# Kernel tuning notes

Hardware: AMD Instinct MI355X
Metric: run time of the kernel (lower is better)

## Reference

```python
import jax, jax.numpy as jnp
import numpy as np

NUM_HEADS = 16
BIG_NEG = -1e9  # additive mask value for padded keys (fp32)


def setup_inputs() -> dict:
    key = jax.random.key(0)
    ks = jax.random.split(key, 12)
    T, S, B, E = 2048, 2048, 2, 1024
    bound = np.sqrt(6.0 / (E + E))  # xavier_uniform for square E x E weights
    inp = {
        'query': jax.random.normal(ks[0], (T, B, E), jnp.float32),
        'key': jax.random.normal(ks[1], (S, B, E), jnp.float32),
        'value': jax.random.normal(ks[2], (S, B, E), jnp.float32),
        'attn_mask': jax.random.normal(ks[3], (T, S), jnp.float32) * 0.1,
        'key_padding_mask': jnp.zeros((B, S), dtype=bool),
        'Wq': jax.random.uniform(ks[4], (E, E), jnp.float32, -bound, bound),
        'bq': jnp.zeros((E,), jnp.float32),
        'Wk': jax.random.uniform(ks[5], (E, E), jnp.float32, -bound, bound),
        'bk': jnp.zeros((E,), jnp.float32),
        'Wv': jax.random.uniform(ks[6], (E, E), jnp.float32, -bound, bound),
        'bv': jnp.zeros((E,), jnp.float32),
        'Wo': jax.random.uniform(ks[7], (E, E), jnp.float32, -bound, bound),
        'bo': jnp.zeros((E,), jnp.float32),
    }
    return inp


def reference(query, key, value, attn_mask, key_padding_mask,
              Wq, bq, Wk, bk, Wv, bv, Wo, bo):
    T, B, E = query.shape
    S = key.shape[0]
    H = NUM_HEADS
    d = E // H
    scale = 1.0 / jnp.sqrt(jnp.asarray(d, query.dtype))

    # projections (nn.Linear: x @ W.T + b), then split heads
    q = (query @ Wq.T + bq).reshape(T, B, H, d) * scale  # [T,B,H,d]
    k = (key @ Wk.T + bk).reshape(S, B, H, d)            # [S,B,H,d]
    v = (value @ Wv.T + bv).reshape(S, B, H, d)          # [S,B,H,d]

    # QK^T scores: [B,H,T,S]
    scores = jnp.einsum('tbhd,sbhd->bhts', q, k)

    # merge masks: additive attn_mask + key_padding_mask (True -> -inf)
    merged = attn_mask[None, None, :, :] + jnp.where(
        key_padding_mask[:, None, None, :], BIG_NEG, 0.0).astype(scores.dtype)
    scores = scores + merged

    attn = jax.nn.softmax(scores, axis=-1)  # dropout p=0 -> identity

    out = jnp.einsum('bhts,sbhd->tbhd', attn, v).reshape(T, B, E)
    return out @ Wo.T + bo  # [T,B,E]
```

## Files before the change

### kernel.cpp

```cpp
#include <hip/hip_runtime.h>
#include <hip/hip_bf16.h>

typedef unsigned short u16;
typedef __attribute__((ext_vector_type(8))) short bf16x8;
typedef __attribute__((ext_vector_type(4))) float f32x4;

#define T_DIM 2048
#define S_DIM 2048
#define B_DIM 2
#define E_DIM 1024
#define H_DIM 16
#define D_HEAD 64
#define NTOK 4096

#if __has_builtin(__builtin_amdgcn_exp2f)
#define EXP2F(x) __builtin_amdgcn_exp2f(x)
#else
#define EXP2F(x) exp2f(x)
#endif

__device__ __forceinline__ float bf2f(u16 u) {
  union { unsigned int i; float f; } v; v.i = ((unsigned int)u) << 16; return v.f;
}
__device__ __forceinline__ u16 f2bf(float f) {
  union { float f; unsigned int i; } v; v.f = f;
  unsigned int r = v.i + 0x7fffu + ((v.i >> 16) & 1u);
  return (u16)(r >> 16);
}
__device__ __forceinline__ unsigned pk2(float a, float b) {
  return (unsigned)f2bf(a) | ((unsigned)f2bf(b) << 16);
}
__device__ __forceinline__ float bfu_lo(unsigned w) {
  union { unsigned int i; float f; } v; v.i = w << 16; return v.f;
}
__device__ __forceinline__ float bfu_hi(unsigned w) {
  union { unsigned int i; float f; } v; v.i = w & 0xffff0000u; return v.f;
}
__device__ __forceinline__ uint4 loadA8(const void* A, size_t base, int bf) {
  if (bf) return *(const uint4*)&((const u16*)A)[base];
  const float* af = (const float*)A + base;
  uint4 r;
  r.x = pk2(af[0], af[1]); r.y = pk2(af[2], af[3]);
  r.z = pk2(af[4], af[5]); r.w = pk2(af[6], af[7]);
  return r;
}

__global__ void detect_dtype(const u16* q, int* flag) {
  int lane = threadIdx.x;
  float v = bf2f(q[2 * lane]);
  bool ok = (v < 16.f) && (v > -16.f);
  unsigned long long b = __ballot(ok);
  if (lane == 0) *flag = (b == ~0ull) ? 1 : 0;
}

__global__ void prep_params(const void* Wq, const void* Wk, const void* Wv, const void* Wo,
                            const void* bq, const void* bk, const void* bv, const void* bo,
                            u16* wqkv, u16* wo, float* b3, float* bof,
                            const int* flag) {
  const int bf = *flag;
  const int W = E_DIM * E_DIM;
  int idx = blockIdx.x * 256 + threadIdx.x;
  if (idx < 4 * W) {
    int which = idx / W, i = idx - which * W;
    const void* src = which == 0 ? Wq : which == 1 ? Wk : which == 2 ? Wv : Wo;
    float v = bf ? bf2f(((const u16*)src)[i]) : ((const float*)src)[i];
    if (which == 0) v *= 0.125f;
    if (which < 3) wqkv[idx] = f2bf(v);
    else           wo[i] = f2bf(v);
  } else {
    int j = idx - 4 * W;
    if (j < 4 * E_DIM) {
      int which = j / E_DIM, i = j - which * E_DIM;
      const void* src = which == 0 ? bq : which == 1 ? bk : which == 2 ? bv : bo;
      float v = bf ? bf2f(((const u16*)src)[i]) : ((const float*)src)[i];
      if (which == 0) v *= 0.125f;
      if (which < 3) b3[j] = v;
      else           bof[i] = v;
    }
  }
}

__launch_bounds__(256)
__global__ void conv_in(const void* __restrict__ Q, const void* __restrict__ K,
                        const void* __restrict__ V,
                        u16* __restrict__ qb, u16* __restrict__ kb,
                        u16* __restrict__ vb, const int* __restrict__ flag) {
  const int bf = *flag;
  const size_t W = (size_t)NTOK * E_DIM;
  size_t e8 = ((size_t)blockIdx.x * 256 + threadIdx.x) * 8;
  int which = (int)(e8 / W);
  size_t i = e8 - (size_t)which * W;
  const void* src = which == 0 ? Q : which == 1 ? K : V;
  u16* dst = which == 0 ? qb : which == 1 ? kb : vb;
  *(uint4*)&dst[i] = loadA8(src, i, bf);
}

__global__ void prep_mask(const void* mask, const unsigned char* kpm,
                          u16* Mc, const int* flag) {
  const float L2E = 1.44269504f;
  const int bf = *flag;
  size_t e8 = ((size_t)blockIdx.x * 256 + threadIdx.x) * 8;
  int b = (int)(e8 / ((size_t)T_DIM * S_DIM));
  size_t rem = e8 - (size_t)b * T_DIM * S_DIM;
  int t = (int)(rem / S_DIM), s = (int)(rem - (size_t)t * S_DIM);
  const unsigned char* kb = &kpm[(size_t)b * S_DIM + s];
  uint4 o;
  if (bf) {
    const u16* m8 = &((const u16*)mask)[(size_t)t * S_DIM + s];
    o.x = pk2((bf2f(m8[0]) + (kb[0] ? -1e9f : 0.f)) * L2E,
              (bf2f(m8[1]) + (kb[1] ? -1e9f : 0.f)) * L2E);
    o.y = pk2((bf2f(m8[2]) + (kb[2] ? -1e9f : 0.f)) * L2E,
              (bf2f(m8[3]) + (kb[3] ? -1e9f : 0.f)) * L2E);
    o.z = pk2((bf2f(m8[4]) + (kb[4] ? -1e9f : 0.f)) * L2E,
              (bf2f(m8[5]) + (kb[5] ? -1e9f : 0.f)) * L2E);
    o.w = pk2((bf2f(m8[6]) + (kb[6] ? -1e9f : 0.f)) * L2E,
              (bf2f(m8[7]) + (kb[7] ? -1e9f : 0.f)) * L2E);
  } else {
    const float* mf = (const float*)mask + (size_t)t * S_DIM + s;
    o.x = pk2((mf[0] + (kb[0] ? -1e9f : 0.f)) * L2E,
              (mf[1] + (kb[1] ? -1e9f : 0.f)) * L2E);
    o.y = pk2((mf[2] + (kb[2] ? -1e9f : 0.f)) * L2E,
              (mf[3] + (kb[3] ? -1e9f : 0.f)) * L2E);
    o.z = pk2((mf[4] + (kb[4] ? -1e9f : 0.f)) * L2E,
              (mf[5] + (kb[5] ? -1e9f : 0.f)) * L2E);
    o.w = pk2((mf[6] + (kb[6] ? -1e9f : 0.f)) * L2E,
              (mf[7] + (kb[7] ? -1e9f : 0.f)) * L2E);
  }
  *(uint4*)&Mc[e8] = o;
}

__launch_bounds__(256)
__global__ void transpose_v(const u16* __restrict__ vp, u16* __restrict__ vt) {
  __shared__ unsigned int t[64 * 65];
  const int tid = threadIdx.x;
  const int s0 = blockIdx.x * 64;
  const int bh = blockIdx.y;
  const int b = bh / H_DIM, h = bh % H_DIM;
  {
    int sr = tid >> 2, cq = (tid & 3) * 16;
    const u16* src = &vp[((size_t)(s0 + sr) * B_DIM + b) * E_DIM + h * 64 + cq];
#pragma unroll
    for (int j = 0; j < 16; j++) t[(cq + j) * 65 + sr] = src[j];
  }
  __syncthreads();
  {
    int d = tid >> 2, sq = (tid & 3) * 16;
    u16* dst = &vt[((size_t)bh * 64 + d) * S_DIM + s0 + sq];
    uint4 o0, o1;
    o0.x = (t[d*65+sq+0] & 0xffffu) | (t[d*65+sq+1] << 16);
    o0.y = (t[d*65+sq+2] & 0xffffu) | (t[d*65+sq+3] << 16);
    o0.z = (t[d*65+sq+4] & 0xffffu) | (t[d*65+sq+5] << 16);
    o0.w = (t[d*65+sq+6] & 0xffffu) | (t[d*65+sq+7] << 16);
    o1.x = (t[d*65+sq+8] & 0xffffu) | (t[d*65+sq+9] << 16);
    o1.y = (t[d*65+sq+10] & 0xffffu) | (t[d*65+sq+11] << 16);
    o1.z = (t[d*65+sq+12] & 0xffffu) | (t[d*65+sq+13] << 16);
    o1.w = (t[d*65+sq+14] & 0xffffu) | (t[d*65+sq+15] << 16);
    *(uint4*)&dst[0] = o0;
    *(uint4*)&dst[8] = o1;
  }
}

__launch_bounds__(256, 2)
__global__ void gemm_qkv(const u16* __restrict__ Qb2, const u16* __restrict__ Kb2,
                         const u16* __restrict__ Vb2, const u16* __restrict__ W3,
                         const float* __restrict__ b3,
                         u16* __restrict__ qp, u16* __restrict__ kp, u16* __restrict__ vp) {
  __shared__ alignas(16) u16 As[128 * 72];
  __shared__ alignas(16) u16 Bs[128 * 72];
  const int tid = threadIdx.x;
  const int wave = tid >> 6, lane = tid & 63;
  const int g = lane >> 4, c = lane & 15;
  const int wy = wave >> 1, wx = wave & 1;
  const int which = blockIdx.x >> 3;
  const u16* A = which == 0 ? Qb2 : which == 1 ? Kb2 : Vb2;
  u16* dst = which == 0 ? qp : which == 1 ? kp : vp;
  const int m0 = blockIdx.y * 128, n0 = blockIdx.x * 128;
  const int K = E_DIM;
  const int rr = tid >> 3, oo = (tid & 7) * 8;

  uint4 pa0, pa1, pa2, pa3, pb0, pb1, pb2, pb3;
  pa0 = *(const uint4*)&A[(size_t)(m0 + rr)      * K + oo];
  pa1 = *(const uint4*)&A[(size_t)(m0 + rr + 32) * K + oo];
  pa2 = *(const uint4*)&A[(size_t)(m0 + rr + 64) * K + oo];
  pa3 = *(const uint4*)&A[(size_t)(m0 + rr + 96) * K + oo];
  pb0 = *(const uint4*)&W3[(size_t)(n0 + rr)      * K + oo];
  pb1 = *(const uint4*)&W3[(size_t)(n0 + rr + 32) * K + oo];
  pb2 = *(const uint4*)&W3[(size_t)(n0 + rr + 64) * K + oo];
  pb3 = *(const uint4*)&W3[(size_t)(n0 + rr + 96) * K + oo];

  f32x4 acc[4][4] = {};
  for (int kc = 0; kc < K; kc += 64) {
    *(uint4*)&As[(rr)      * 72 + oo] = pa0;
    *(uint4*)&As[(rr + 32) * 72 + oo] = pa1;
    *(uint4*)&As[(rr + 64) * 72 + oo] = pa2;
    *(uint4*)&As[(rr + 96) * 72 + oo] = pa3;
    *(uint4*)&Bs[(rr)      * 72 + oo] = pb0;
    *(uint4*)&Bs[(rr + 32) * 72 + oo] = pb1;
    *(uint4*)&Bs[(rr + 64) * 72 + oo] = pb2;
    *(uint4*)&Bs[(rr + 96) * 72 + oo] = pb3;
    __syncthreads();
    if (kc + 64 < K) {
      int k2 = kc + 64;
      pa0 = *(const uint4*)&A[(size_t)(m0 + rr)      * K + k2 + oo];
      pa1 = *(const uint4*)&A[(size_t)(m0 + rr + 32) * K + k2 + oo];
      pa2 = *(const uint4*)&A[(size_t)(m0 + rr + 64) * K + k2 + oo];
      pa3 = *(const uint4*)&A[(size_t)(m0 + rr + 96) * K + k2 + oo];
      pb0 = *(const uint4*)&W3[(size_t)(n0 + rr)      * K + k2 + oo];
      pb1 = *(const uint4*)&W3[(size_t)(n0 + rr + 32) * K + k2 + oo];
      pb2 = *(const uint4*)&W3[(size_t)(n0 + rr + 64) * K + k2 + oo];
      pb3 = *(const uint4*)&W3[(size_t)(n0 + rr + 96) * K + k2 + oo];
    }
#pragma unroll
    for (int ks = 0; ks < 2; ks++) {
      bf16x8 av0 = *(const bf16x8*)&As[(wy * 64 + 0 * 16 + c) * 72 + ks * 32 + g * 8];
      bf16x8 av1 = *(const bf16x8*)&As[(wy * 64 + 1 * 16 + c) * 72 + ks * 32 + g * 8];
      bf16x8 av2 = *(const bf16x8*)&As[(wy * 64 + 2 * 16 + c) * 72 + ks * 32 + g * 8];
      bf16x8 av3 = *(const bf16x8*)&As[(wy * 64 + 3 * 16 + c) * 72 + ks * 32 + g * 8];
      bf16x8 bv0 = *(const bf16x8*)&Bs[(wx * 64 + 0 * 16 + c) * 72 + ks * 32 + g * 8];
      bf16x8 bv1 = *(const bf16x8*)&Bs[(wx * 64 + 1 * 16 + c) * 72 + ks * 32 + g * 8];
      bf16x8 bv2 = *(const bf16x8*)&Bs[(wx * 64 + 2 * 16 + c) * 72 + ks * 32 + g * 8];
      bf16x8 bv3 = *(const bf16x8*)&Bs[(wx * 64 + 3 * 16 + c) * 72 + ks * 32 + g * 8];
      acc[0][0] = __builtin_amdgcn_mfma_f32_16x16x32_bf16(av0, bv0, acc[0][0], 0, 0, 0);
      acc[0][1] = __builtin_amdgcn_mfma_f32_16x16x32_bf16(av0, bv1, acc[0][1], 0, 0, 0);
      acc[0][2] = __builtin_amdgcn_mfma_f32_16x16x32_bf16(av0, bv2, acc[0][2], 0, 0, 0);
      acc[0][3] = __builtin_amdgcn_mfma_f32_16x16x32_bf16(av0, bv3, acc[0][3], 0, 0, 0);
      acc[1][0] = __builtin_amdgcn_mfma_f32_16x16x32_bf16(av1, bv0, acc[1][0], 0, 0, 0);
      acc[1][1] = __builtin_amdgcn_mfma_f32_16x16x32_bf16(av1, bv1, acc[1][1], 0, 0, 0);
      acc[1][2] = __builtin_amdgcn_mfma_f32_16x16x32_bf16(av1, bv2, acc[1][2], 0, 0, 0);
      acc[1][3] = __builtin_amdgcn_mfma_f32_16x16x32_bf16(av1, bv3, acc[1][3], 0, 0, 0);
      acc[2][0] = __builtin_amdgcn_mfma_f32_16x16x32_bf16(av2, bv0, acc[2][0], 0, 0, 0);
      acc[2][1] = __builtin_amdgcn_mfma_f32_16x16x32_bf16(av2, bv1, acc[2][1], 0, 0, 0);
      acc[2][2] = __builtin_amdgcn_mfma_f32_16x16x32_bf16(av2, bv2, acc[2][2], 0, 0, 0);
      acc[2][3] = __builtin_amdgcn_mfma_f32_16x16x32_bf16(av2, bv3, acc[2][3], 0, 0, 0);
      acc[3][0] = __builtin_amdgcn_mfma_f32_16x16x32_bf16(av3, bv0, acc[3][0], 0, 0, 0);
      acc[3][1] = __builtin_amdgcn_mfma_f32_16x16x32_bf16(av3, bv1, acc[3][1], 0, 0, 0);
      acc[3][2] = __builtin_amdgcn_mfma_f32_16x16x32_bf16(av3, bv2, acc[3][2], 0, 0, 0);
      acc[3][3] = __builtin_amdgcn_mfma_f32_16x16x32_bf16(av3, bv3, acc[3][3], 0, 0, 0);
    }
    __syncthreads();
  }
#pragma unroll
  for (int mi = 0; mi < 4; mi++)
#pragma unroll
    for (int ni = 0; ni < 4; ni++)
#pragma unroll
      for (int r = 0; r < 4; r++) {
        int row = m0 + wy * 64 + mi * 16 + g * 4 + r;
        int col = n0 + wx * 64 + ni * 16 + c;
        int inner = col & (E_DIM - 1);
        dst[(size_t)row * E_DIM + inner] = f2bf(acc[mi][ni][r] + b3[col]);
      }
}

__launch_bounds__(256, 2)
__global__ void gemm_o(const u16* __restrict__ A, const u16* __restrict__ Bw,
                       const float* __restrict__ bias, void* __restrict__ C,
                       int out_f32) {
  __shared__ alignas(16) u16 As[64 * 72];
  __shared__ alignas(16) u16 Bs[128 * 72];
  const int tid = threadIdx.x;
  const int wave = tid >> 6, lane = tid & 63;
  const int g = lane >> 4, c = lane & 15;
  const int wy = wave >> 1, wx = wave & 1;
  const int m0 = blockIdx.y * 64, n0 = blockIdx.x * 128;
  const int K = E_DIM, N = E_DIM;
  const int rr = tid >> 3, oo = (tid & 7) * 8;

  uint4 pa0, pa1, pb0, pb1, pb2, pb3;
  pa0 = *(const uint4*)&A[(size_t)(m0 + rr)      * K + oo];
  pa1 = *(const uint4*)&A[(size_t)(m0 + rr + 32) * K + oo];
  pb0 = *(const uint4*)&Bw[(size_t)(n0 + rr)      * K + oo];
  pb1 = *(const uint4*)&Bw[(size_t)(n0 + rr + 32) * K + oo];
  pb2 = *(const uint4*)&Bw[(size_t)(n0 + rr + 64) * K + oo];
  pb3 = *(const uint4*)&Bw[(size_t)(n0 + rr + 96) * K + oo];

  f32x4 acc[2][4] = {};
  for (int kc = 0; kc < K; kc += 64) {
    *(uint4*)&As[(rr)      * 72 + oo] = pa0;
    *(uint4*)&As[(rr + 32) * 72 + oo] = pa1;
    *(uint4*)&Bs[(rr)      * 72 + oo] = pb0;
    *(uint4*)&Bs[(rr + 32) * 72 + oo] = pb1;
    *(uint4*)&Bs[(rr + 64) * 72 + oo] = pb2;
    *(uint4*)&Bs[(rr + 96) * 72 + oo] = pb3;
    __syncthreads();
    if (kc + 64 < K) {
      int k2 = kc + 64;
      pa0 = *(const uint4*)&A[(size_t)(m0 + rr)      * K + k2 + oo];
      pa1 = *(const uint4*)&A[(size_t)(m0 + rr + 32) * K + k2 + oo];
      pb0 = *(const uint4*)&Bw[(size_t)(n0 + rr)      * K + k2 + oo];
      pb1 = *(const uint4*)&Bw[(size_t)(n0 + rr + 32) * K + k2 + oo];
      pb2 = *(const uint4*)&Bw[(size_t)(n0 + rr + 64) * K + k2 + oo];
      pb3 = *(const uint4*)&Bw[(size_t)(n0 + rr + 96) * K + k2 + oo];
    }
#pragma unroll
    for (int ks = 0; ks < 2; ks++) {
      bf16x8 av0 = *(const bf16x8*)&As[(wy * 32 + 0 * 16 + c) * 72 + ks * 32 + g * 8];
      bf16x8 av1 = *(const bf16x8*)&As[(wy * 32 + 1 * 16 + c) * 72 + ks * 32 + g * 8];
      bf16x8 bv0 = *(const bf16x8*)&Bs[(wx * 64 + 0 * 16 + c) * 72 + ks * 32 + g * 8];
      bf16x8 bv1 = *(const bf16x8*)&Bs[(wx * 64 + 1 * 16 + c) * 72 + ks * 32 + g * 8];
      bf16x8 bv2 = *(const bf16x8*)&Bs[(wx * 64 + 2 * 16 + c) * 72 + ks * 32 + g * 8];
      bf16x8 bv3 = *(const bf16x8*)&Bs[(wx * 64 + 3 * 16 + c) * 72 + ks * 32 + g * 8];
      acc[0][0] = __builtin_amdgcn_mfma_f32_16x16x32_bf16(av0, bv0, acc[0][0], 0, 0, 0);
      acc[0][1] = __builtin_amdgcn_mfma_f32_16x16x32_bf16(av0, bv1, acc[0][1], 0, 0, 0);
      acc[0][2] = __builtin_amdgcn_mfma_f32_16x16x32_bf16(av0, bv2, acc[0][2], 0, 0, 0);
      acc[0][3] = __builtin_amdgcn_mfma_f32_16x16x32_bf16(av0, bv3, acc[0][3], 0, 0, 0);
      acc[1][0] = __builtin_amdgcn_mfma_f32_16x16x32_bf16(av1, bv0, acc[1][0], 0, 0, 0);
      acc[1][1] = __builtin_amdgcn_mfma_f32_16x16x32_bf16(av1, bv1, acc[1][1], 0, 0, 0);
      acc[1][2] = __builtin_amdgcn_mfma_f32_16x16x32_bf16(av1, bv2, acc[1][2], 0, 0, 0);
      acc[1][3] = __builtin_amdgcn_mfma_f32_16x16x32_bf16(av1, bv3, acc[1][3], 0, 0, 0);
    }
    __syncthreads();
  }
#pragma unroll
  for (int mi = 0; mi < 2; mi++)
#pragma unroll
    for (int ni = 0; ni < 4; ni++)
#pragma unroll
      for (int r = 0; r < 4; r++) {
        int row = m0 + wy * 32 + mi * 16 + g * 4 + r;
        int col = n0 + wx * 64 + ni * 16 + c;
        float v = acc[mi][ni][r] + bias[col];
        size_t idx = (size_t)row * N + col;
        if (out_f32) ((float*)C)[idx] = v;
        else         ((u16*)C)[idx] = f2bf(v);
      }
}

__launch_bounds__(256, 4)
__global__ void flash_attn(const u16* __restrict__ Qb, const u16* __restrict__ Kb,
                           const u16* __restrict__ Vtg, const u16* __restrict__ Mc,
                           u16* __restrict__ ctx) {
  __shared__ alignas(16) u16 Ks[64 * 72];
  __shared__ alignas(16) u16 Vs[64 * 72];
  __shared__ alignas(16) u16 MP[64 * 72];
  const int tid = threadIdx.x;
  const int wave = tid >> 6, lane = tid & 63;
  const int g = lane >> 4, c = lane & 15;
  const int bh = blockIdx.x;
  const int t0 = blockIdx.y * 64;
  const int b = bh / H_DIM, h = bh % H_DIM;
  const size_t hoff = (size_t)h * D_HEAD;
  const float L2E = 1.44269504f;
  const u16* mc = &Mc[((size_t)b * T_DIM + t0) * S_DIM];
  const int rr = tid >> 3, oo = (tid & 7) * 8;

  *(uint4*)&Ks[(rr)      * 72 + oo] =
      *(const uint4*)&Qb[((size_t)(t0 + rr)      * B_DIM + b) * E_DIM + hoff + oo];
  *(uint4*)&Ks[(rr + 32) * 72 + oo] =
      *(const uint4*)&Qb[((size_t)(t0 + rr + 32) * B_DIM + b) * E_DIM + hoff + oo];
  __syncthreads();
  const int arow = wave * 16 + c;
  bf16x8 q0 = *(const bf16x8*)&Ks[arow * 72 + g * 8];
  bf16x8 q1 = *(const bf16x8*)&Ks[arow * 72 + 32 + g * 8];

  uint4 pk0, pk1, pv0, pv1, pm0, pm1;
  pk0 = *(const uint4*)&Kb[((size_t)(rr)      * B_DIM + b) * E_DIM + hoff + oo];
  pk1 = *(const uint4*)&Kb[((size_t)(rr + 32) * B_DIM + b) * E_DIM + hoff + oo];
  pv0 = *(const uint4*)&Vtg[((size_t)bh * 64 + rr)      * S_DIM + oo];
  pv1 = *(const uint4*)&Vtg[((size_t)bh * 64 + rr + 32) * S_DIM + oo];
  pm0 = *(const uint4*)&mc[(size_t)(rr)      * S_DIM + oo];
  pm1 = *(const uint4*)&mc[(size_t)(rr + 32) * S_DIM + oo];
  __syncthreads();

  f32x4 O[4] = {};
  float rsum = 0.f;
  const int trow = arow * 72;

  for (int s0 = 0; s0 < S_DIM; s0 += 64) {
    *(uint4*)&Ks[(rr)      * 72 + oo] = pk0;
    *(uint4*)&Ks[(rr + 32) * 72 + oo] = pk1;
    *(uint4*)&Vs[(rr)      * 72 + oo] = pv0;
    *(uint4*)&Vs[(rr + 32) * 72 + oo] = pv1;
    *(uint4*)&MP[(rr)      * 72 + oo] = pm0;
    *(uint4*)&MP[(rr + 32) * 72 + oo] = pm1;
    __syncthreads();
    if (s0 + 64 < S_DIM) {
      int s2 = s0 + 64;
      pk0 = *(const uint4*)&Kb[((size_t)(s2 + rr)      * B_DIM + b) * E_DIM + hoff + oo];
      pk1 = *(const uint4*)&Kb[((size_t)(s2 + rr + 32) * B_DIM + b) * E_DIM + hoff + oo];
      pv0 = *(const uint4*)&Vtg[((size_t)bh * 64 + rr)      * S_DIM + s2 + oo];
      pv1 = *(const uint4*)&Vtg[((size_t)bh * 64 + rr + 32) * S_DIM + s2 + oo];
      pm0 = *(const uint4*)&mc[(size_t)(rr)      * S_DIM + s2 + oo];
      pm1 = *(const uint4*)&mc[(size_t)(rr + 32) * S_DIM + s2 + oo];
    }

    f32x4 sc[4] = {};
#pragma unroll
    for (int n = 0; n < 4; n++) {
      bf16x8 k0 = *(const bf16x8*)&Ks[(n * 16 + c) * 72 + g * 8];
      bf16x8 k1 = *(const bf16x8*)&Ks[(n * 16 + c) * 72 + 32 + g * 8];
      sc[n] = __builtin_amdgcn_mfma_f32_16x16x32_bf16(k0, q0, sc[n], 0, 0, 0);
      sc[n] = __builtin_amdgcn_mfma_f32_16x16x32_bf16(k1, q1, sc[n], 0, 0, 0);
    }
#pragma unroll
    for (int n = 0; n < 4; n++) {
      uint2 mw = *(const uint2*)&MP[trow + n * 16 + g * 4];
      float p0 = EXP2F(fmaf(sc[n][0], L2E, bfu_lo(mw.x)));
      float p1 = EXP2F(fmaf(sc[n][1], L2E, bfu_hi(mw.x)));
      float p2 = EXP2F(fmaf(sc[n][2], L2E, bfu_lo(mw.y)));
      float p3 = EXP2F(fmaf(sc[n][3], L2E, bfu_hi(mw.y)));
      rsum += (p0 + p1) + (p2 + p3);
      *(unsigned*)&MP[trow + n * 16 + g * 4]     = pk2(p0, p1);
      *(unsigned*)&MP[trow + n * 16 + g * 4 + 2] = pk2(p2, p3);
    }
    bf16x8 p0 = *(const bf16x8*)&MP[arow * 72 + g * 8];
    bf16x8 p1 = *(const bf16x8*)&MP[arow * 72 + 32 + g * 8];
#pragma unroll
    for (int n = 0; n < 4; n++) {
      bf16x8 v0 = *(const bf16x8*)&Vs[(n * 16 + c) * 72 + g * 8];
      bf16x8 v1 = *(const bf16x8*)&Vs[(n * 16 + c) * 72 + 32 + g * 8];
      O[n] = __builtin_amdgcn_mfma_f32_16x16x32_bf16(p0, v0, O[n], 0, 0, 0);
      O[n] = __builtin_amdgcn_mfma_f32_16x16x32_bf16(p1, v1, O[n], 0, 0, 0);
    }
    __syncthreads();
  }
  float l = rsum;
  l += __shfl_xor(l, 16, 64);
  l += __shfl_xor(l, 32, 64);
  float rl = 1.f / l;
#pragma unroll
  for (int r = 0; r < 4; r++) {
    float rlr = __shfl(rl, g * 4 + r, 64);
    int t = t0 + wave * 16 + g * 4 + r;
#pragma unroll
    for (int n = 0; n < 4; n++) {
      int dcol = n * 16 + c;
      ctx[((size_t)t * B_DIM + b) * E_DIM + hoff + dcol] = f2bf(O[n][r] * rlr);
    }
  }
}

extern "C" void kernel_launch(void* const* d_in, const int* in_sizes, int n_in,
                              void* d_out, int out_size, void* d_ws, size_t ws_size,
                              hipStream_t stream) {
  const void* query = d_in[0];
  const void* key   = d_in[1];
  const void* value = d_in[2];
  const void* amask = d_in[3];
  const unsigned char* kpm = (const unsigned char*)d_in[4];
  const void* Wq = d_in[5];  const void* bq = d_in[6];
  const void* Wk = d_in[7];  const void* bk = d_in[8];
  const void* Wv = d_in[9];  const void* bv = d_in[10];
  const void* Wo = d_in[11]; const void* bo = d_in[12];

  int out_f32 = 0;
  {
    hipDeviceptr_t base = nullptr; size_t sz = 0;
    if (hipMemGetAddressRange(&base, &sz, (hipDeviceptr_t)d_out) == hipSuccess && sz) {
      size_t avail = sz - (size_t)((char*)d_out - (char*)base);
      size_t need_f32 = (size_t)out_size * 4;
      if (avail >= need_f32 && avail <= need_f32 + need_f32 / 2) out_f32 = 1;
    }
  }

  char* ws = (char*)d_ws;
  size_t off = 0;
  auto alloc = [&](size_t bytes) {
    void* p = ws + off;
    off += (bytes + 255) & ~(size_t)255;
    return p;
  };
  int*   flag = (int*)  alloc(256);
  u16*   qp   = (u16*)  alloc((size_t)NTOK * E_DIM * 2);
  u16*   kp   = (u16*)  alloc((size_t)NTOK * E_DIM * 2);
  u16*   vp   = (u16*)  alloc((size_t)NTOK * E_DIM * 2);
  u16*   vt   = (u16*)  alloc((size_t)NTOK * E_DIM * 2);
  u16*   Mcb  = (u16*)  alloc((size_t)B_DIM * T_DIM * S_DIM * 2);
  u16*   wqkv = (u16*)  alloc((size_t)3 * E_DIM * E_DIM * 2);
  u16*   wo   = (u16*)  alloc((size_t)E_DIM * E_DIM * 2);
  float* b3   = (float*)alloc(3 * E_DIM * 4);
  float* bof  = (float*)alloc(E_DIM * 4);
  if (off > ws_size) return;

  u16* qb  = vt;
  u16* kb2 = Mcb;
  u16* vb2 = Mcb + (size_t)NTOK * E_DIM;

  detect_dtype<<<1, 64, 0, stream>>>((const u16*)query, flag);

  {
    int total = 4 * E_DIM * E_DIM + 4 * E_DIM;
    prep_params<<<(total + 255) / 256, 256, 0, stream>>>(
        Wq, Wk, Wv, Wo, bq, bk, bv, bo, wqkv, wo, b3, bof, flag);
  }

  {
    size_t total8 = (size_t)3 * NTOK * E_DIM / 8;
    conv_in<<<(unsigned)(total8 / 256), 256, 0, stream>>>(
        query, key, value, qb, kb2, vb2, flag);
  }

  gemm_qkv<<<dim3(3 * E_DIM / 128, NTOK / 128), 256, 0, stream>>>(
      qb, kb2, vb2, wqkv, b3, qp, kp, vp);

  {
    size_t total8 = (size_t)B_DIM * T_DIM * S_DIM / 8;
    prep_mask<<<(unsigned)(total8 / 256), 256, 0, stream>>>(amask, kpm, Mcb, flag);
  }

  transpose_v<<<dim3(S_DIM / 64, B_DIM * H_DIM), 256, 0, stream>>>(vp, vt);

  u16* ctx = vp;
  flash_attn<<<dim3(B_DIM * H_DIM, T_DIM / 64), 256, 0, stream>>>(qp, kp, vt, Mcb, ctx);

  gemm_o<<<dim3(E_DIM / 128, NTOK / 64), 256, 0, stream>>>(ctx, wo, bof, d_out, out_f32);
}
```

Baseline: 284.5 us.

## Load GEMM tiles directly into LDS with XOR-swizzled layout

The QKV and output-projection GEMMs stop staging tiles through registers and instead use global_load_lds to copy 16-byte chunks straight from global memory into shared memory. The padded stride-72 LDS layout is replaced by an unpadded stride-64 layout with an XOR swizzle on the 8-element column block, to avoid bank conflicts on the MFMA fragment reads. The register prefetch of the next tile is gone, so loads are no longer overlapped with compute within a block; the QKV kernel raises its occupancy hint from 2 to 3 blocks per CU to hide that latency with more resident waves.

```diff
diff --git a/kernel.cpp b/kernel.cpp
--- a/kernel.cpp
+++ b/kernel.cpp
@@ -18,6 +18,8 @@
 #else
 #define EXP2F(x) exp2f(x)
 #endif
+
+#define GLL16(gp, lp) __builtin_amdgcn_global_load_lds((gp), (lp), 16, 0, 0)
 
 __device__ __forceinline__ float bf2f(u16 u) {
   union { unsigned int i; float f; } v; v.i = ((unsigned int)u) << 16; return v.f;
@@ -160,13 +162,13 @@
   }
 }
 
-__launch_bounds__(256, 2)
+__launch_bounds__(256, 3)
 __global__ void gemm_qkv(const u16* __restrict__ Qb2, const u16* __restrict__ Kb2,
                          const u16* __restrict__ Vb2, const u16* __restrict__ W3,
                          const float* __restrict__ b3,
                          u16* __restrict__ qp, u16* __restrict__ kp, u16* __restrict__ vp) {
-  __shared__ alignas(16) u16 As[128 * 72];
-  __shared__ alignas(16) u16 Bs[128 * 72];
+  __shared__ alignas(16) u16 As[128 * 64];
+  __shared__ alignas(16) u16 Bs[128 * 64];
   const int tid = threadIdx.x;
   const int wave = tid >> 6, lane = tid & 63;
   const int g = lane >> 4, c = lane & 15;
@@ -176,50 +178,31 @@
   u16* dst = which == 0 ? qp : which == 1 ? kp : vp;
   const int m0 = blockIdx.y * 128, n0 = blockIdx.x * 128;
   const int K = E_DIM;
-  const int rr = tid >> 3, oo = (tid & 7) * 8;
-
-  uint4 pa0, pa1, pa2, pa3, pb0, pb1, pb2, pb3;
-  pa0 = *(const uint4*)&A[(size_t)(m0 + rr)      * K + oo];
-  pa1 = *(const uint4*)&A[(size_t)(m0 + rr + 32) * K + oo];
-  pa2 = *(const uint4*)&A[(size_t)(m0 + rr + 64) * K + oo];
-  pa3 = *(const uint4*)&A[(size_t)(m0 + rr + 96) * K + oo];
-  pb0 = *(const uint4*)&W3[(size_t)(n0 + rr)      * K + oo];
-  pb1 = *(const uint4*)&W3[(size_t)(n0 + rr + 32) * K + oo];
-  pb2 = *(const uint4*)&W3[(size_t)(n0 + rr + 64) * K + oo];
-  pb3 = *(const uint4*)&W3[(size_t)(n0 + rr + 96) * K + oo];
+
+  const int swr = lane >> 3;
+  const int swb = (lane & 7) ^ swr;
+  const u16* Ag = &A [(size_t)(m0 + wave * 8 + swr) * K + swb * 8];
+  const u16* Bg = &W3[(size_t)(n0 + wave * 8 + swr) * K + swb * 8];
 
   f32x4 acc[4][4] = {};
   for (int kc = 0; kc < K; kc += 64) {
-    *(uint4*)&As[(rr)      * 72 + oo] = pa0;
-    *(uint4*)&As[(rr + 32) * 72 + oo] = pa1;
-    *(uint4*)&As[(rr + 64) * 72 + oo] = pa2;
-    *(uint4*)&As[(rr + 96) * 72 + oo] = pa3;
-    *(uint4*)&Bs[(rr)      * 72 + oo] = pb0;
-    *(uint4*)&Bs[(rr + 32) * 72 + oo] = pb1;
-    *(uint4*)&Bs[(rr + 64) * 72 + oo] = pb2;
-    *(uint4*)&Bs[(rr + 96) * 72 + oo] = pb3;
-    __syncthreads();
-    if (kc + 64 < K) {
-      int k2 = kc + 64;
-      pa0 = *(const uint4*)&A[(size_t)(m0 + rr)      * K + k2 + oo];
-      pa1 = *(const uint4*)&A[(size_t)(m0 + rr + 32) * K + k2 + oo];
-      pa2 = *(const uint4*)&A[(size_t)(m0 + rr + 64) * K + k2 + oo];
-      pa3 = *(const uint4*)&A[(size_t)(m0 + rr + 96) * K + k2 + oo];
-      pb0 = *(const uint4*)&W3[(size_t)(n0 + rr)      * K + k2 + oo];
-      pb1 = *(const uint4*)&W3[(size_t)(n0 + rr + 32) * K + k2 + oo];
-      pb2 = *(const uint4*)&W3[(size_t)(n0 + rr + 64) * K + k2 + oo];
-      pb3 = *(const uint4*)&W3[(size_t)(n0 + rr + 96) * K + k2 + oo];
-    }
+#pragma unroll
+    for (int i = 0; i < 4; i++) {
+      GLL16(&Ag[(size_t)(i * 32) * K + kc], &As[(wave * 8 + i * 32) * 64]);
+      GLL16(&Bg[(size_t)(i * 32) * K + kc], &Bs[(wave * 8 + i * 32) * 64]);
+    }
+    __syncthreads();
 #pragma unroll
     for (int ks = 0; ks < 2; ks++) {
-      bf16x8 av0 = *(const bf16x8*)&As[(wy * 64 + 0 * 16 + c) * 72 + ks * 32 + g * 8];
-      bf16x8 av1 = *(const bf16x8*)&As[(wy * 64 + 1 * 16 + c) * 72 + ks * 32 + g * 8];
-      bf16x8 av2 = *(const bf16x8*)&As[(wy * 64 + 2 * 16 + c) * 72 + ks * 32 + g * 8];
-      bf16x8 av3 = *(const bf16x8*)&As[(wy * 64 + 3 * 16 + c) * 72 + ks * 32 + g * 8];
-      bf16x8 bv0 = *(const bf16x8*)&Bs[(wx * 64 + 0 * 16 + c) * 72 + ks * 32 + g * 8];
-      bf16x8 bv1 = *(const bf16x8*)&Bs[(wx * 64 + 1 * 16 + c) * 72 + ks * 32 + g * 8];
-      bf16x8 bv2 = *(const bf16x8*)&Bs[(wx * 64 + 2 * 16 + c) * 72 + ks * 32 + g * 8];
-      bf16x8 bv3 = *(const bf16x8*)&Bs[(wx * 64 + 3 * 16 + c) * 72 + ks * 32 + g * 8];
+      const int kb = (((ks << 2) | g) ^ (c & 7)) * 8;
+      bf16x8 av0 = *(const bf16x8*)&As[(wy * 64 +  0 + c) * 64 + kb];
+      bf16x8 av1 = *(const bf16x8*)&As[(wy * 64 + 16 + c) * 64 + kb];
+      bf16x8 av2 = *(const bf16x8*)&As[(wy * 64 + 32 + c) * 64 + kb];
+      bf16x8 av3 = *(const bf16x8*)&As[(wy * 64 + 48 + c) * 64 + kb];
+      bf16x8 bv0 = *(const bf16x8*)&Bs[(wx * 64 +  0 + c) * 64 + kb];
+      bf16x8 bv1 = *(const bf16x8*)&Bs[(wx * 64 + 16 + c) * 64 + kb];
+      bf16x8 bv2 = *(const bf16x8*)&Bs[(wx * 64 + 32 + c) * 64 + kb];
+      bf16x8 bv3 = *(const bf16x8*)&Bs[(wx * 64 + 48 + c) * 64 + kb];
       acc[0][0] = __builtin_amdgcn_mfma_f32_16x16x32_bf16(av0, bv0, acc[0][0], 0, 0, 0);
       acc[0][1] = __builtin_amdgcn_mfma_f32_16x16x32_bf16(av0, bv1, acc[0][1], 0, 0, 0);
       acc[0][2] = __builtin_amdgcn_mfma_f32_16x16x32_bf16(av0, bv2, acc[0][2], 0, 0, 0);
@@ -253,53 +236,41 @@
 }
 
 __launch_bounds__(256, 2)
-__global__ void gemm_o(const u16* __restrict__ A, const u16* __restrict__ Bw,
+__global__ void gemm_o(const u16* __restrict__ Aa, const u16* __restrict__ Bw,
                        const float* __restrict__ bias, void* __restrict__ C,
                        int out_f32) {
-  __shared__ alignas(16) u16 As[64 * 72];
-  __shared__ alignas(16) u16 Bs[128 * 72];
+  __shared__ alignas(16) u16 As[64 * 64];
+  __shared__ alignas(16) u16 Bs[128 * 64];
   const int tid = threadIdx.x;
   const int wave = tid >> 6, lane = tid & 63;
   const int g = lane >> 4, c = lane & 15;
   const int wy = wave >> 1, wx = wave & 1;
   const int m0 = blockIdx.y * 64, n0 = blockIdx.x * 128;
   const int K = E_DIM, N = E_DIM;
-  const int rr = tid >> 3, oo = (tid & 7) * 8;
-
-  uint4 pa0, pa1, pb0, pb1, pb2, pb3;
-  pa0 = *(const uint4*)&A[(size_t)(m0 + rr)      * K + oo];
-  pa1 = *(const uint4*)&A[(size_t)(m0 + rr + 32) * K + oo];
-  pb0 = *(const uint4*)&Bw[(size_t)(n0 + rr)      * K + oo];
-  pb1 = *(const uint4*)&Bw[(size_t)(n0 + rr + 32) * K + oo];
-  pb2 = *(const uint4*)&Bw[(size_t)(n0 + rr + 64) * K + oo];
-  pb3 = *(const uint4*)&Bw[(size_t)(n0 + rr + 96) * K + oo];
+
+  const int swr = lane >> 3;
+  const int swb = (lane & 7) ^ swr;
+  const u16* Ag = &Aa[(size_t)(m0 + wave * 8 + swr) * K + swb * 8];
+  const u16* Bg = &Bw[(size_t)(n0 + wave * 8 + swr) * K + swb * 8];
 
   f32x4 acc[2][4] = {};
   for (int kc = 0; kc < K; kc += 64) {
-    *(uint4*)&As[(rr)      * 72 + oo] = pa0;
-    *(uint4*)&As[(rr + 32) * 72 + oo] = pa1;
-    *(uint4*)&Bs[(rr)      * 72 + oo] = pb0;
-    *(uint4*)&Bs[(rr + 32) * 72 + oo] = pb1;
-    *(uint4*)&Bs[(rr + 64) * 72 + oo] = pb2;
-    *(uint4*)&Bs[(rr + 96) * 72 + oo] = pb3;
-    __syncthreads();
-    if (kc + 64 < K) {
-      int k2 = kc + 64;
-      pa0 = *(const uint4*)&A[(size_t)(m0 + rr)      * K + k2 + oo];
-      pa1 = *(const uint4*)&A[(size_t)(m0 + rr + 32) * K + k2 + oo];
-      pb0 = *(const uint4*)&Bw[(size_t)(n0 + rr)      * K + k2 + oo];
-      pb1 = *(const uint4*)&Bw[(size_t)(n0 + rr + 32) * K + k2 + oo];
-      pb2 = *(const uint4*)&Bw[(size_t)(n0 + rr + 64) * K + k2 + oo];
-      pb3 = *(const uint4*)&Bw[(size_t)(n0 + rr + 96) * K + k2 + oo];
-    }
+#pragma unroll
+    for (int i = 0; i < 2; i++)
+      GLL16(&Ag[(size_t)(i * 32) * K + kc], &As[(wave * 8 + i * 32) * 64]);
+#pragma unroll
+    for (int i = 0; i < 4; i++)
+      GLL16(&Bg[(size_t)(i * 32) * K + kc], &Bs[(wave * 8 + i * 32) * 64]);
+    __syncthreads();
 #pragma unroll
     for (int ks = 0; ks < 2; ks++) {
-      bf16x8 av0 = *(const bf16x8*)&As[(wy * 32 + 0 * 16 + c) * 72 + ks * 32 + g * 8];
-      bf16x8 av1 = *(const bf16x8*)&As[(wy * 32 + 1 * 16 + c) * 72 + ks * 32 + g * 8];
-      bf16x8 bv0 = *(const bf16x8*)&Bs[(wx * 64 + 0 * 16 + c) * 72 + ks * 32 + g * 8];
-      bf16x8 bv1 = *(const bf16x8*)&Bs[(wx * 64 + 1 * 16 + c) * 72 + ks * 32 + g * 8];
-      bf16x8 bv2 = *(const bf16x8*)&Bs[(wx * 64 + 2 * 16 + c) * 72 + ks * 32 + g * 8];
-      bf16x8 bv3 = *(const bf16x8*)&Bs[(wx * 64 + 3 * 16 + c) * 72 + ks * 32 + g * 8];
+      const int kb = (((ks << 2) | g) ^ (c & 7)) * 8;
+      bf16x8 av0 = *(const bf16x8*)&As[(wy * 32 +  0 + c) * 64 + kb];
+      bf16x8 av1 = *(const bf16x8*)&As[(wy * 32 + 16 + c) * 64 + kb];
+      bf16x8 bv0 = *(const bf16x8*)&Bs[(wx * 64 +  0 + c) * 64 + kb];
+      bf16x8 bv1 = *(const bf16x8*)&Bs[(wx * 64 + 16 + c) * 64 + kb];
+      bf16x8 bv2 = *(const bf16x8*)&Bs[(wx * 64 + 32 + c) * 64 + kb];
+      bf16x8 bv3 = *(const bf16x8*)&Bs[(wx * 64 + 48 + c) * 64 + kb];
       acc[0][0] = __builtin_amdgcn_mfma_f32_16x16x32_bf16(av0, bv0, acc[0][0], 0, 0, 0);
       acc[0][1] = __builtin_amdgcn_mfma_f32_16x16x32_bf16(av0, bv1, acc[0][1], 0, 0, 0);
       acc[0][2] = __builtin_amdgcn_mfma_f32_16x16x32_bf16(av0, bv2, acc[0][2], 0, 0, 0);
```

New measurement: 286.3 us. Within noise of the previous version (+0.6%).
